# Kernel optimization log

Hardware: AMD Instinct MI355X
Metric: run time of the kernel (lower is better)

Reference implementation:

```python
import jax, jax.numpy as jnp
import numpy as np

COMMITMENT = 0.25  # beta


def setup_inputs() -> dict:
    key = jax.random.key(0)
    k1, k2 = jax.random.split(key)
    B, M, D, K = 16, 4096, 64, 1024
    z_e = jax.random.normal(k1, (B, M, D), dtype=jnp.float32)
    embed = jax.random.normal(k2, (K, D), dtype=jnp.float32)  # codebook C in R^{KxD}
    return {"z_e": z_e, "embed": embed}


def reference(z_e, embed):
    """Eval-mode VQ forward: nearest-code lookup + VQ loss + straight-through.

    z_e:   (B, M, D) encoder outputs
    embed: (K, D) codebook
    Returns (z_q_st, indices, vq_loss).
    """
    B, M, D = z_e.shape
    flat = z_e.reshape(-1, D)  # (N, D)
    dist = (
        jnp.sum(flat * flat, axis=1, keepdims=True)
        - 2.0 * (flat @ embed.T)
        + jnp.sum(embed * embed, axis=1)[None, :]
    )
    indices = jnp.argmin(dist, axis=1)  # (N,)
    z_q = embed[indices].reshape(B, M, D)  # gather

    sg = jax.lax.stop_gradient
    codebook_loss = jnp.mean((z_q - sg(z_e)) ** 2)
    commitment_loss = jnp.mean((z_e - sg(z_q)) ** 2)
    vq_loss = codebook_loss + COMMITMENT * commitment_loss

    z_q_st = z_e + sg(z_q - z_e)  # straight-through estimator
    return z_q_st, indices.reshape(B, M), vq_loss
```

## Files before the change

kernel.cpp:

```cpp
#include <hip/hip_runtime.h>
#include <hip/hip_bf16.h>
#include <stdint.h>

#define D_     64
#define K_     1024
#define N_     65536
#define TK     256
#define TPB    256
#define RPW    32
#define RPB    128
#define NBLK   (N_ / RPB)
#define MARGIN 0.06f

typedef __bf16 bf16x8 __attribute__((ext_vector_type(8)));
typedef float  f32x4  __attribute__((ext_vector_type(4)));

__device__ __forceinline__ unsigned short bf16_rne(float f) {
    union { float f; uint32_t u; } v; v.f = f;
    const uint32_t u = v.u;
    return (unsigned short)((u + 0x7fffu + ((u >> 16) & 1u)) >> 16);
}
__device__ __forceinline__ float bf16_tof(unsigned short h) {
    union { uint32_t u; float f; } v; v.u = ((uint32_t)h) << 16;
    return v.f;
}
__device__ __forceinline__ __bf16 bits_bf16(unsigned short u) {
    union { unsigned short u; __bf16 h; } v; v.u = u; return v.h;
}

__global__ __launch_bounds__(256) void vq_prep(const float* __restrict__ embed,
                                               double* __restrict__ n64,
                                               float* __restrict__ n32,
                                               unsigned short* __restrict__ ehg,
                                               unsigned short* __restrict__ elg) {
    const int k = blockIdx.x * 256 + threadIdx.x;
    const float4* e4 = (const float4*)(embed + (size_t)k * D_);
    double acc = 0.0;
#pragma unroll
    for (int q = 0; q < 16; ++q) {
        const float4 e = e4[q];
        float c[4] = {e.x, e.y, e.z, e.w};
        ushort4 h4, l4;
        unsigned short hb[4], lb[4];
#pragma unroll
        for (int j = 0; j < 4; ++j) {
            hb[j] = bf16_rne(c[j]);
            lb[j] = bf16_rne(c[j] - bf16_tof(hb[j]));
            acc = fma((double)c[j], (double)c[j], acc);
        }
        h4.x = hb[0]; h4.y = hb[1]; h4.z = hb[2]; h4.w = hb[3];
        l4.x = lb[0]; l4.y = lb[1]; l4.z = lb[2]; l4.w = lb[3];
        *(ushort4*)(ehg + (size_t)k * D_ + q * 4) = h4;
        *(ushort4*)(elg + (size_t)k * D_ + q * 4) = l4;
    }
    n64[k] = acc;
    n32[k] = (float)acc;
}

__global__ __launch_bounds__(TPB, 2) void vq_main(const float* __restrict__ z_e,
                                                  const float* __restrict__ embed,
                                                  const unsigned short* __restrict__ ehg,
                                                  const unsigned short* __restrict__ elg,
                                                  const float* __restrict__ n32g,
                                                  const double* __restrict__ n64g,
                                                  float* __restrict__ out,
                                                  float* __restrict__ partials) {
    __shared__ float4 lds_eh[TK * 8];
    __shared__ float4 lds_el[TK * 8];
    __shared__ float  lds_n[TK];
    __shared__ float  red[TPB];

    const int tid  = threadIdx.x;
    const int lane = tid & 63;
    const int w    = tid >> 6;
    const int lg   = lane >> 4;
    const int lc   = lane & 15;
    const int wrow0 = blockIdx.x * RPB + w * RPW;

    float  xs[2][16];
    bf16x8 ah[2][2], al[2][2];
#pragma unroll
    for (int t = 0; t < 2; ++t) {
        const int row = wrow0 + t * 16 + lc;
        const float4* xg = (const float4*)(z_e + (size_t)row * D_ + lg * 16);
#pragma unroll
        for (int q = 0; q < 4; ++q) {
            const float4 x = xg[q];
            xs[t][q * 4 + 0] = x.x; xs[t][q * 4 + 1] = x.y;
            xs[t][q * 4 + 2] = x.z; xs[t][q * 4 + 3] = x.w;
        }
#pragma unroll
        for (int s = 0; s < 2; ++s) {
#pragma unroll
            for (int i = 0; i < 8; ++i) {
                const float xf = xs[t][s * 8 + i];
                const unsigned short hb = bf16_rne(xf);
                const unsigned short lb = bf16_rne(xf - bf16_tof(hb));
                ah[t][s][i] = bits_bf16(hb);
                al[t][s][i] = bits_bf16(lb);
            }
        }
    }

    float b1[2][4], b2[2][4];
    int   i1[2][4];
#pragma unroll
    for (int t = 0; t < 2; ++t)
#pragma unroll
        for (int rg = 0; rg < 4; ++rg) { b1[t][rg] = 3.4e38f; b2[t][rg] = 3.4e38f; i1[t][rg] = 0; }

    for (int kt = 0; kt < K_; kt += TK) {
        __syncthreads();
        {
            const float4* sh = (const float4*)(ehg + (size_t)kt * D_);
            const float4* sl = (const float4*)(elg + (size_t)kt * D_);
#pragma unroll
            for (int it = 0; it < 8; ++it) {
                const int m  = tid + it * TPB;
                const int sw = (m * 16) ^ ((((m * 16) >> 7) & 7) << 4);
                lds_eh[sw >> 4] = sh[m];
                lds_el[sw >> 4] = sl[m];
            }
            lds_n[tid] = n32g[kt + tid];
        }
        __syncthreads();

#pragma unroll 4
        for (int ct = 0; ct < TK / 16; ++ct) {
            const int cl = ct * 16 + lc;
            const int a0 = (cl * 128 + lg * 32) ^ ((cl & 7) << 4);
            const bf16x8 bh0 = *(const bf16x8*)((const char*)lds_eh + a0);
            const bf16x8 bh1 = *(const bf16x8*)((const char*)lds_eh + (a0 ^ 16));
            const bf16x8 bl0 = *(const bf16x8*)((const char*)lds_el + a0);
            const bf16x8 bl1 = *(const bf16x8*)((const char*)lds_el + (a0 ^ 16));
            const float  nv  = lds_n[cl];
            const int    ki  = kt + cl;
#pragma unroll
            for (int t = 0; t < 2; ++t) {
                f32x4 acc = {0.f, 0.f, 0.f, 0.f};
                acc = __builtin_amdgcn_mfma_f32_16x16x32_bf16(ah[t][0], bh0, acc, 0, 0, 0);
                acc = __builtin_amdgcn_mfma_f32_16x16x32_bf16(ah[t][1], bh1, acc, 0, 0, 0);
                acc = __builtin_amdgcn_mfma_f32_16x16x32_bf16(ah[t][0], bl0, acc, 0, 0, 0);
                acc = __builtin_amdgcn_mfma_f32_16x16x32_bf16(ah[t][1], bl1, acc, 0, 0, 0);
                acc = __builtin_amdgcn_mfma_f32_16x16x32_bf16(al[t][0], bh0, acc, 0, 0, 0);
                acc = __builtin_amdgcn_mfma_f32_16x16x32_bf16(al[t][1], bh1, acc, 0, 0, 0);
#pragma unroll
                for (int rg = 0; rg < 4; ++rg) {
                    const float s = fmaf(-2.0f, acc[rg], nv);
                    if (s < b1[t][rg])      { b2[t][rg] = b1[t][rg]; b1[t][rg] = s; i1[t][rg] = ki; }
                    else if (s < b2[t][rg]) { b2[t][rg] = s; }
                }
            }
        }
    }

#pragma unroll
    for (int t = 0; t < 2; ++t)
#pragma unroll
        for (int rg = 0; rg < 4; ++rg)
#pragma unroll
            for (int off = 1; off <= 8; off <<= 1) {
                const float ob1 = __shfl_xor(b1[t][rg], off);
                const float ob2 = __shfl_xor(b2[t][rg], off);
                const int   oi1 = __shfl_xor(i1[t][rg], off);
                if (ob1 < b1[t][rg] || (ob1 == b1[t][rg] && oi1 < i1[t][rg])) {
                    b2[t][rg] = fminf(b1[t][rg], ob2); b1[t][rg] = ob1; i1[t][rg] = oi1;
                } else {
                    b2[t][rg] = fminf(ob1, b2[t][rg]);
                }
            }

#pragma unroll
    for (int t = 0; t < 2; ++t) {
#pragma unroll
        for (int rg = 0; rg < 4; ++rg) {
            for (int g = 0; g < 4; ++g) {
                const float g1 = __shfl(b1[t][rg], g << 4);
                const float g2 = __shfl(b2[t][rg], g << 4);
                if (g2 - g1 < MARGIN) {
                    const int grow = wrow0 + t * 16 + g * 4 + rg;
                    const float* xp = z_e + (size_t)grow * D_;
                    double bs = 1.0e300; int bi = 1 << 30;
                    for (int c0 = 0; c0 < K_; c0 += 64) {
                        const int c = c0 + lane;
                        const float* ep = embed + (size_t)c * D_;
                        double dot = 0.0;
#pragma unroll
                        for (int j = 0; j < D_; ++j)
                            dot = fma((double)xp[j], (double)ep[j], dot);
                        const double sc = fma(-2.0, dot, n64g[c]);
                        if (sc < bs) { bs = sc; bi = c; }
                    }
#pragma unroll
                    for (int off = 32; off > 0; off >>= 1) {
                        const double so = __shfl_xor(bs, off);
                        const int    io = __shfl_xor(bi, off);
                        if (so < bs || (so == bs && io < bi)) { bs = so; bi = io; }
                    }
                    if (lg == g) i1[t][rg] = bi;
                }
            }
        }
    }

    float sq = 0.f;
#pragma unroll
    for (int t = 0; t < 2; ++t) {
        const int srcl = (lc >> 2) << 4;
        const int c0v = __shfl(i1[t][0], srcl);
        const int c1v = __shfl(i1[t][1], srcl);
        const int c2v = __shfl(i1[t][2], srcl);
        const int c3v = __shfl(i1[t][3], srcl);
        const int rsel = lc & 3;
        int bidx = (rsel == 0) ? c0v : (rsel == 1) ? c1v : (rsel == 2) ? c2v : c3v;
        bidx &= (K_ - 1);
        const int row = wrow0 + t * 16 + lc;
        const float4* eg = (const float4*)(embed + (size_t)bidx * D_ + lg * 16);
        float4*       og = (float4*)(out + (size_t)row * D_ + lg * 16);
#pragma unroll
        for (int q = 0; q < 4; ++q) {
            const float4 e = eg[q];
            const int   x0 = q * 4;
            const float d0 = e.x - xs[t][x0 + 0];
            const float d1 = e.y - xs[t][x0 + 1];
            const float d2 = e.z - xs[t][x0 + 2];
            const float d3 = e.w - xs[t][x0 + 3];
            sq = fmaf(d0, d0, sq); sq = fmaf(d1, d1, sq);
            sq = fmaf(d2, d2, sq); sq = fmaf(d3, d3, sq);
            float4 o;
            o.x = xs[t][x0 + 0] + d0;
            o.y = xs[t][x0 + 1] + d1;
            o.z = xs[t][x0 + 2] + d2;
            o.w = xs[t][x0 + 3] + d3;
            og[q] = o;
        }
        if (lg == 0) out[(size_t)N_ * D_ + row] = (float)bidx;
    }

    red[tid] = sq;
    __syncthreads();
#pragma unroll
    for (int s = TPB / 2; s > 0; s >>= 1) {
        if (tid < s) red[tid] += red[tid + s];
        __syncthreads();
    }
    if (tid == 0) partials[blockIdx.x] = red[0];
}

__global__ __launch_bounds__(256) void vq_loss_final(const float* __restrict__ partials,
                                                     float* __restrict__ out) {
    __shared__ float red[256];
    const int tid = threadIdx.x;
    float s = 0.f;
#pragma unroll
    for (int i = 0; i < NBLK / 256; ++i) s += partials[tid + i * 256];
    red[tid] = s;
    __syncthreads();
#pragma unroll
    for (int w = 128; w > 0; w >>= 1) {
        if (tid < w) red[tid] += red[tid + w];
        __syncthreads();
    }
    if (tid == 0)
        out[(size_t)N_ * D_ + N_] = 1.25f * red[0] / (float)((size_t)N_ * D_);
}

extern "C" void kernel_launch(void* const* d_in, const int* in_sizes, int n_in,
                              void* d_out, int out_size, void* d_ws, size_t ws_size,
                              hipStream_t stream) {
    const float* z_e;
    const float* embed;
    if (in_sizes[0] == N_ * D_) {
        z_e   = (const float*)d_in[0];
        embed = (const float*)d_in[1];
    } else {
        z_e   = (const float*)d_in[1];
        embed = (const float*)d_in[0];
    }
    float* out = (float*)d_out;

    double* n64           = (double*)d_ws;
    float*  n32           = (float*)(n64 + K_);
    float*  partials      = n32 + K_;
    unsigned short* ehg   = (unsigned short*)(partials + NBLK);
    unsigned short* elg   = ehg + (size_t)K_ * D_;

    vq_prep<<<K_ / 256, 256, 0, stream>>>(embed, n64, n32, ehg, elg);
    vq_main<<<NBLK, TPB, 0, stream>>>(z_e, embed, ehg, elg, n32, n64, out, partials);
    vq_loss_final<<<1, 256, 0, stream>>>(partials, out);
}
```

Baseline: 218.0 us.

## Halve rows per wave, shrink K tile, split MFMA chains, go branchless

Each wave now handles 16 rows instead of 32 and the codebook tile shrinks from 256 to 128 codes. This cuts registers and LDS so the main kernel can run 4 blocks per CU instead of 2. The six bf16 MFMAs per tile are split into two independent accumulator chains to shorten dependency stalls. Codebook norms are kept in registers, the top-2 tracking becomes branchless selects, the reduction buffer reuses the tile LDS, and the prep kernel uses 64-thread blocks. The cost is that each LDS codebook fragment now feeds half as many MFMAs, so LDS traffic per flop rises.

```diff
diff --git a/kernel.cpp b/kernel.cpp
--- a/kernel.cpp
+++ b/kernel.cpp
@@ -5,10 +5,9 @@
 #define D_     64
 #define K_     1024
 #define N_     65536
-#define TK     256
+#define TK     128
 #define TPB    256
-#define RPW    32
-#define RPB    128
+#define RPB    64
 #define NBLK   (N_ / RPB)
 #define MARGIN 0.06f
 
@@ -28,12 +27,12 @@
     union { unsigned short u; __bf16 h; } v; v.u = u; return v.h;
 }
 
-__global__ __launch_bounds__(256) void vq_prep(const float* __restrict__ embed,
-                                               double* __restrict__ n64,
-                                               float* __restrict__ n32,
-                                               unsigned short* __restrict__ ehg,
-                                               unsigned short* __restrict__ elg) {
-    const int k = blockIdx.x * 256 + threadIdx.x;
+__global__ __launch_bounds__(64) void vq_prep(const float* __restrict__ embed,
+                                              double* __restrict__ n64,
+                                              float* __restrict__ n32,
+                                              unsigned short* __restrict__ ehg,
+                                              unsigned short* __restrict__ elg) {
+    const int k = blockIdx.x * 64 + threadIdx.x;
     const float4* e4 = (const float4*)(embed + (size_t)k * D_);
     double acc = 0.0;
 #pragma unroll
@@ -57,7 +56,7 @@
     n32[k] = (float)acc;
 }
 
-__global__ __launch_bounds__(TPB, 2) void vq_main(const float* __restrict__ z_e,
+__global__ __launch_bounds__(TPB, 4) void vq_main(const float* __restrict__ z_e,
                                                   const float* __restrict__ embed,
                                                   const unsigned short* __restrict__ ehg,
                                                   const unsigned short* __restrict__ elg,
@@ -67,65 +66,62 @@
                                                   float* __restrict__ partials) {
     __shared__ float4 lds_eh[TK * 8];
     __shared__ float4 lds_el[TK * 8];
-    __shared__ float  lds_n[TK];
-    __shared__ float  red[TPB];
 
     const int tid  = threadIdx.x;
     const int lane = tid & 63;
     const int w    = tid >> 6;
     const int lg   = lane >> 4;
     const int lc   = lane & 15;
-    const int wrow0 = blockIdx.x * RPB + w * RPW;
-
-    float  xs[2][16];
-    bf16x8 ah[2][2], al[2][2];
-#pragma unroll
-    for (int t = 0; t < 2; ++t) {
-        const int row = wrow0 + t * 16 + lc;
+    const int wrow0 = blockIdx.x * RPB + w * 16;
+
+    float  xs[16];
+    bf16x8 ah[2], al[2];
+    {
+        const int row = wrow0 + lc;
         const float4* xg = (const float4*)(z_e + (size_t)row * D_ + lg * 16);
 #pragma unroll
         for (int q = 0; q < 4; ++q) {
             const float4 x = xg[q];
-            xs[t][q * 4 + 0] = x.x; xs[t][q * 4 + 1] = x.y;
-            xs[t][q * 4 + 2] = x.z; xs[t][q * 4 + 3] = x.w;
+            xs[q * 4 + 0] = x.x; xs[q * 4 + 1] = x.y;
+            xs[q * 4 + 2] = x.z; xs[q * 4 + 3] = x.w;
         }
 #pragma unroll
         for (int s = 0; s < 2; ++s) {
 #pragma unroll
             for (int i = 0; i < 8; ++i) {
-                const float xf = xs[t][s * 8 + i];
+                const float xf = xs[s * 8 + i];
                 const unsigned short hb = bf16_rne(xf);
                 const unsigned short lb = bf16_rne(xf - bf16_tof(hb));
-                ah[t][s][i] = bits_bf16(hb);
-                al[t][s][i] = bits_bf16(lb);
-            }
-        }
-    }
-
-    float b1[2][4], b2[2][4];
-    int   i1[2][4];
-#pragma unroll
-    for (int t = 0; t < 2; ++t)
-#pragma unroll
-        for (int rg = 0; rg < 4; ++rg) { b1[t][rg] = 3.4e38f; b2[t][rg] = 3.4e38f; i1[t][rg] = 0; }
+                ah[s][i] = bits_bf16(hb);
+                al[s][i] = bits_bf16(lb);
+            }
+        }
+    }
+
+    float b1[4], b2[4];
+    int   i1[4];
+#pragma unroll
+    for (int rg = 0; rg < 4; ++rg) { b1[rg] = 3.4e38f; b2[rg] = 3.4e38f; i1[rg] = 0; }
 
     for (int kt = 0; kt < K_; kt += TK) {
         __syncthreads();
+        float nreg[8];
         {
             const float4* sh = (const float4*)(ehg + (size_t)kt * D_);
             const float4* sl = (const float4*)(elg + (size_t)kt * D_);
 #pragma unroll
-            for (int it = 0; it < 8; ++it) {
+            for (int it = 0; it < 4; ++it) {
                 const int m  = tid + it * TPB;
                 const int sw = (m * 16) ^ ((((m * 16) >> 7) & 7) << 4);
                 lds_eh[sw >> 4] = sh[m];
                 lds_el[sw >> 4] = sl[m];
             }
-            lds_n[tid] = n32g[kt + tid];
-        }
-        __syncthreads();
-
-#pragma unroll 4
+#pragma unroll
+            for (int ct = 0; ct < 8; ++ct) nreg[ct] = n32g[kt + ct * 16 + lc];
+        }
+        __syncthreads();
+
+#pragma unroll
         for (int ct = 0; ct < TK / 16; ++ct) {
             const int cl = ct * 16 + lc;
             const int a0 = (cl * 128 + lg * 32) ^ ((cl & 7) << 4);
@@ -133,110 +129,106 @@
             const bf16x8 bh1 = *(const bf16x8*)((const char*)lds_eh + (a0 ^ 16));
             const bf16x8 bl0 = *(const bf16x8*)((const char*)lds_el + a0);
             const bf16x8 bl1 = *(const bf16x8*)((const char*)lds_el + (a0 ^ 16));
-            const float  nv  = lds_n[cl];
-            const int    ki  = kt + cl;
-#pragma unroll
-            for (int t = 0; t < 2; ++t) {
-                f32x4 acc = {0.f, 0.f, 0.f, 0.f};
-                acc = __builtin_amdgcn_mfma_f32_16x16x32_bf16(ah[t][0], bh0, acc, 0, 0, 0);
-                acc = __builtin_amdgcn_mfma_f32_16x16x32_bf16(ah[t][1], bh1, acc, 0, 0, 0);
-                acc = __builtin_amdgcn_mfma_f32_16x16x32_bf16(ah[t][0], bl0, acc, 0, 0, 0);
-                acc = __builtin_amdgcn_mfma_f32_16x16x32_bf16(ah[t][1], bl1, acc, 0, 0, 0);
-                acc = __builtin_amdgcn_mfma_f32_16x16x32_bf16(al[t][0], bh0, acc, 0, 0, 0);
-                acc = __builtin_amdgcn_mfma_f32_16x16x32_bf16(al[t][1], bh1, acc, 0, 0, 0);
-#pragma unroll
-                for (int rg = 0; rg < 4; ++rg) {
-                    const float s = fmaf(-2.0f, acc[rg], nv);
-                    if (s < b1[t][rg])      { b2[t][rg] = b1[t][rg]; b1[t][rg] = s; i1[t][rg] = ki; }
-                    else if (s < b2[t][rg]) { b2[t][rg] = s; }
+            f32x4 acc0 = {0.f, 0.f, 0.f, 0.f};
+            f32x4 acc1 = {0.f, 0.f, 0.f, 0.f};
+            acc0 = __builtin_amdgcn_mfma_f32_16x16x32_bf16(ah[0], bh0, acc0, 0, 0, 0);
+            acc1 = __builtin_amdgcn_mfma_f32_16x16x32_bf16(ah[1], bh1, acc1, 0, 0, 0);
+            acc0 = __builtin_amdgcn_mfma_f32_16x16x32_bf16(al[0], bh0, acc0, 0, 0, 0);
+            acc1 = __builtin_amdgcn_mfma_f32_16x16x32_bf16(al[1], bh1, acc1, 0, 0, 0);
+            acc0 = __builtin_amdgcn_mfma_f32_16x16x32_bf16(ah[0], bl0, acc0, 0, 0, 0);
+            acc1 = __builtin_amdgcn_mfma_f32_16x16x32_bf16(ah[1], bl1, acc1, 0, 0, 0);
+            const int ki = kt + cl;
+#pragma unroll
+            for (int rg = 0; rg < 4; ++rg) {
+                const float s  = fmaf(-2.0f, acc0[rg] + acc1[rg], nreg[ct]);
+                const bool  lt = s < b1[rg];
+                const float m2 = fminf(s, b2[rg]);
+                b2[rg] = lt ? b1[rg] : m2;
+                b1[rg] = lt ? s      : b1[rg];
+                i1[rg] = lt ? ki     : i1[rg];
+            }
+        }
+    }
+
+#pragma unroll
+    for (int rg = 0; rg < 4; ++rg)
+#pragma unroll
+        for (int off = 1; off <= 8; off <<= 1) {
+            const float ob1 = __shfl_xor(b1[rg], off);
+            const float ob2 = __shfl_xor(b2[rg], off);
+            const int   oi1 = __shfl_xor(i1[rg], off);
+            if (ob1 < b1[rg] || (ob1 == b1[rg] && oi1 < i1[rg])) {
+                b2[rg] = fminf(b1[rg], ob2); b1[rg] = ob1; i1[rg] = oi1;
+            } else {
+                b2[rg] = fminf(ob1, b2[rg]);
+            }
+        }
+
+#pragma unroll
+    for (int rg = 0; rg < 4; ++rg) {
+        for (int g = 0; g < 4; ++g) {
+            const float g1 = __shfl(b1[rg], g << 4);
+            const float g2 = __shfl(b2[rg], g << 4);
+            if (g2 - g1 < MARGIN) {
+                const int grow = wrow0 + g * 4 + rg;
+                const float* xp = z_e + (size_t)grow * D_;
+                double bs = 1.0e300; int bi = 1 << 30;
+                for (int c0 = 0; c0 < K_; c0 += 64) {
+                    const int c = c0 + lane;
+                    const float* ep = embed + (size_t)c * D_;
+                    double dot = 0.0;
+#pragma unroll
+                    for (int j = 0; j < D_; ++j)
+                        dot = fma((double)xp[j], (double)ep[j], dot);
+                    const double sc = fma(-2.0, dot, n64g[c]);
+                    if (sc < bs) { bs = sc; bi = c; }
                 }
-            }
-        }
-    }
-
-#pragma unroll
-    for (int t = 0; t < 2; ++t)
-#pragma unroll
-        for (int rg = 0; rg < 4; ++rg)
-#pragma unroll
-            for (int off = 1; off <= 8; off <<= 1) {
-                const float ob1 = __shfl_xor(b1[t][rg], off);
-                const float ob2 = __shfl_xor(b2[t][rg], off);
-                const int   oi1 = __shfl_xor(i1[t][rg], off);
-                if (ob1 < b1[t][rg] || (ob1 == b1[t][rg] && oi1 < i1[t][rg])) {
-                    b2[t][rg] = fminf(b1[t][rg], ob2); b1[t][rg] = ob1; i1[t][rg] = oi1;
-                } else {
-                    b2[t][rg] = fminf(ob1, b2[t][rg]);
+#pragma unroll
+                for (int off = 32; off > 0; off >>= 1) {
+                    const double so = __shfl_xor(bs, off);
+                    const int    io = __shfl_xor(bi, off);
+                    if (so < bs || (so == bs && io < bi)) { bs = so; bi = io; }
                 }
-            }
-
-#pragma unroll
-    for (int t = 0; t < 2; ++t) {
-#pragma unroll
-        for (int rg = 0; rg < 4; ++rg) {
-            for (int g = 0; g < 4; ++g) {
-                const float g1 = __shfl(b1[t][rg], g << 4);
-                const float g2 = __shfl(b2[t][rg], g << 4);
-                if (g2 - g1 < MARGIN) {
-                    const int grow = wrow0 + t * 16 + g * 4 + rg;
-                    const float* xp = z_e + (size_t)grow * D_;
-                    double bs = 1.0e300; int bi = 1 << 30;
-                    for (int c0 = 0; c0 < K_; c0 += 64) {
-                        const int c = c0 + lane;
-                        const float* ep = embed + (size_t)c * D_;
-                        double dot = 0.0;
-#pragma unroll
-                        for (int j = 0; j < D_; ++j)
-                            dot = fma((double)xp[j], (double)ep[j], dot);
-                        const double sc = fma(-2.0, dot, n64g[c]);
-                        if (sc < bs) { bs = sc; bi = c; }
-                    }
-#pragma unroll
-                    for (int off = 32; off > 0; off >>= 1) {
-                        const double so = __shfl_xor(bs, off);
-                        const int    io = __shfl_xor(bi, off);
-                        if (so < bs || (so == bs && io < bi)) { bs = so; bi = io; }
-                    }
-                    if (lg == g) i1[t][rg] = bi;
-                }
+                if (lg == g) i1[rg] = bi;
             }
         }
     }
 
     float sq = 0.f;
-#pragma unroll
-    for (int t = 0; t < 2; ++t) {
+    {
         const int srcl = (lc >> 2) << 4;
-        const int c0v = __shfl(i1[t][0], srcl);
-        const int c1v = __shfl(i1[t][1], srcl);
-        const int c2v = __shfl(i1[t][2], srcl);
-        const int c3v = __shfl(i1[t][3], srcl);
+        const int c0v = __shfl(i1[0], srcl);
+        const int c1v = __shfl(i1[1], srcl);
+        const int c2v = __shfl(i1[2], srcl);
+        const int c3v = __shfl(i1[3], srcl);
         const int rsel = lc & 3;
         int bidx = (rsel == 0) ? c0v : (rsel == 1) ? c1v : (rsel == 2) ? c2v : c3v;
         bidx &= (K_ - 1);
-        const int row = wrow0 + t * 16 + lc;
+        const int row = wrow0 + lc;
         const float4* eg = (const float4*)(embed + (size_t)bidx * D_ + lg * 16);
         float4*       og = (float4*)(out + (size_t)row * D_ + lg * 16);
 #pragma unroll
         for (int q = 0; q < 4; ++q) {
             const float4 e = eg[q];
             const int   x0 = q * 4;
-            const float d0 = e.x - xs[t][x0 + 0];
-            const float d1 = e.y - xs[t][x0 + 1];
-            const float d2 = e.z - xs[t][x0 + 2];
-            const float d3 = e.w - xs[t][x0 + 3];
+            const float d0 = e.x - xs[x0 + 0];
+            const float d1 = e.y - xs[x0 + 1];
+            const float d2 = e.z - xs[x0 + 2];
+            const float d3 = e.w - xs[x0 + 3];
             sq = fmaf(d0, d0, sq); sq = fmaf(d1, d1, sq);
             sq = fmaf(d2, d2, sq); sq = fmaf(d3, d3, sq);
             float4 o;
-            o.x = xs[t][x0 + 0] + d0;
-            o.y = xs[t][x0 + 1] + d1;
-            o.z = xs[t][x0 + 2] + d2;
-            o.w = xs[t][x0 + 3] + d3;
+            o.x = xs[x0 + 0] + d0;
+            o.y = xs[x0 + 1] + d1;
+            o.z = xs[x0 + 2] + d2;
+            o.w = xs[x0 + 3] + d3;
             og[q] = o;
         }
         if (lg == 0) out[(size_t)N_ * D_ + row] = (float)bidx;
     }
 
+    __syncthreads();
+    float* red = (float*)lds_eh;
     red[tid] = sq;
     __syncthreads();
 #pragma unroll
@@ -285,7 +277,7 @@
     unsigned short* ehg   = (unsigned short*)(partials + NBLK);
     unsigned short* elg   = ehg + (size_t)K_ * D_;
 
-    vq_prep<<<K_ / 256, 256, 0, stream>>>(embed, n64, n32, ehg, elg);
+    vq_prep<<<K_ / 64, 64, 0, stream>>>(embed, n64, n32, ehg, elg);
     vq_main<<<NBLK, TPB, 0, stream>>>(z_e, embed, ehg, elg, n32, n64, out, partials);
     vq_loss_final<<<1, 256, 0, stream>>>(partials, out);
 }
```

Result: slower. 287.1 us (+31.7%).
